# Optimization experiments

Hardware: AMD Instinct MI355X
Metric: run time of the kernel (lower is better)

## Reference

```python
import jax, jax.numpy as jnp
import numpy as np

NEG_SLOPE = 0.01  # torch leaky_relu default

def leaky_relu(x):
    return jnp.where(x >= 0, x, NEG_SLOPE * x)

def setup_inputs() -> dict:
    key = jax.random.key(0)
    ks = jax.random.split(key, 12)
    N, E = 100000, 800000
    C_in, C_edge, pre, H, hs, C_out = 64, 32, 96, 4, 24, 128
    aggr_out = H * hs + 1  # count=True appends in-degree column
    x = jax.random.normal(ks[0], (N, C_in), dtype=jnp.float32)
    edge_attr = jax.random.normal(ks[1], (E, C_edge), dtype=jnp.float32)
    edge_index = jax.random.randint(ks[2], (2, E), 0, N, dtype=jnp.int32)
    s = 0.05
    W_pre = jax.random.normal(ks[3], (C_in + C_edge, pre), dtype=jnp.float32) * s
    b_pre = jax.random.normal(ks[4], (pre,), dtype=jnp.float32) * s
    W_att = jax.random.normal(ks[5], (pre, H), dtype=jnp.float32) * s
    b_att = jax.random.normal(ks[6], (H,), dtype=jnp.float32) * s
    W_val = jax.random.normal(ks[7], (pre, H * hs), dtype=jnp.float32) * s
    b_val = jax.random.normal(ks[8], (H * hs,), dtype=jnp.float32) * s
    W_out = jax.random.normal(ks[9], (C_in + aggr_out, C_out), dtype=jnp.float32) * s
    b_out = jax.random.normal(ks[10], (C_out,), dtype=jnp.float32) * s
    return {"x": x, "edge_attr": edge_attr, "edge_index": edge_index,
            "W_pre": W_pre, "b_pre": b_pre, "W_att": W_att, "b_att": b_att,
            "W_val": W_val, "b_val": b_val, "W_out": W_out, "b_out": b_out}

def reference(x, edge_attr, edge_index, W_pre, b_pre, W_att, b_att, W_val, b_val, W_out, b_out):
    N = x.shape[0]
    src, dst = edge_index[0], edge_index[1]
    H = W_att.shape[1]
    hs = W_val.shape[1] // H
    # gather + pre MLP: [E, in+edge] -> [E, pre]
    msg = jnp.concatenate([x[src], edge_attr], axis=-1)
    msg = leaky_relu(msg @ W_pre + b_pre)
    # multi-head attention aggregation keyed by destination
    logits = msg @ W_att + b_att                       # [E, H]
    vals = (msg @ W_val + b_val).reshape(-1, H, hs)    # [E, H, hs]
    seg_max = jax.ops.segment_max(logits, dst, num_segments=N)      # [N, H]
    seg_max = jnp.where(jnp.isfinite(seg_max), seg_max, 0.0)
    alpha = jnp.exp(logits - seg_max[dst])                          # [E, H]
    denom = jax.ops.segment_sum(alpha, dst, num_segments=N)         # [N, H]
    alpha = alpha / denom[dst]
    agg = jax.ops.segment_sum(alpha[:, :, None] * vals, dst, num_segments=N)  # [N, H, hs]
    agg = agg.reshape(N, H * hs)
    count = jax.ops.segment_sum(jnp.ones((src.shape[0], 1), dtype=x.dtype), dst, num_segments=N)
    messages = jnp.concatenate([agg, count], axis=-1)
    out = jnp.concatenate([x, messages], axis=-1)
    return leaky_relu(out @ W_out + b_out)
```

## Files before the change

### kernel.cpp

```cpp
#include <hip/hip_runtime.h>


#define NEG 0.01f

__device__ __forceinline__ float lrelu(float v) { return v > 0.f ? v : NEG * v; }

__device__ __forceinline__ unsigned bfpack2(float a, float b) {
    unsigned ua = __float_as_uint(a); ua = (ua + 0x7fff + ((ua >> 16) & 1)) >> 16;
    unsigned ub = __float_as_uint(b); ub = (ub + 0x7fff + ((ub >> 16) & 1)) >> 16;
    return ua | (ub << 16);
}

__global__ void zero_kernel(float* __restrict__ p, long n) {
    long i = ((long)blockIdx.x * 256 + threadIdx.x) * 4;
    if (i + 3 < n) {
        *(float4*)(p + i) = make_float4(0.f, 0.f, 0.f, 0.f);
    } else {
        for (long k = i; k < n; ++k) p[k] = 0.f;
    }
}

__global__ void hist_kernel(const int* __restrict__ ei, int* __restrict__ cnt, int E) {
    int e = blockIdx.x * 256 + threadIdx.x;
    if (e < E) atomicAdd(&cnt[ei[E + e]], 1);
}

__global__ __launch_bounds__(1024)
void scan_kernel(const int* __restrict__ cnt, int* __restrict__ offs,
                 int* __restrict__ curs, int N) {
    __shared__ int ls[1024];
    int tid = threadIdx.x;
    int chunk = (N + 1023) >> 10;
    int lo = tid * chunk;
    int hi = lo + chunk; if (hi > N) hi = N; if (lo > N) lo = N;
    int s = 0;
    for (int i = lo; i < hi; ++i) s += cnt[i];
    ls[tid] = s;
    __syncthreads();
    for (int off = 1; off < 1024; off <<= 1) {
        int v = 0;
        if (tid >= off) v = ls[tid - off];
        __syncthreads();
        ls[tid] += v;
        __syncthreads();
    }
    int run = ls[tid] - s;
    for (int i = lo; i < hi; ++i) {
        offs[i] = run; curs[i] = run; run += cnt[i];
    }
}

__global__ __launch_bounds__(256)
void blocksum_kernel(const int* __restrict__ cnt, int* __restrict__ bsum, int N) {
    int base = blockIdx.x * 1024;
    int tid = threadIdx.x;
    int v = 0;
#pragma unroll
    for (int r = 0; r < 4; ++r) {
        int idx = base + r * 256 + tid;
        if (idx < N) v += cnt[idx];
    }
#pragma unroll
    for (int d = 32; d > 0; d >>= 1) v += __shfl_down(v, d, 64);
    __shared__ int ws[4];
    int wv = tid >> 6, lane = tid & 63;
    if (lane == 0) ws[wv] = v;
    __syncthreads();
    if (tid == 0) bsum[blockIdx.x] = ws[0] + ws[1] + ws[2] + ws[3];
}

__global__ __launch_bounds__(1024)
void bscan_kernel(int* __restrict__ bsum, int NB) {
    __shared__ int ls[1024];
    int tid = threadIdx.x;
    int v = (tid < NB) ? bsum[tid] : 0;
    ls[tid] = v;
    __syncthreads();
    for (int off = 1; off < 1024; off <<= 1) {
        int t = 0;
        if (tid >= off) t = ls[tid - off];
        __syncthreads();
        ls[tid] += t;
        __syncthreads();
    }
    if (tid < NB) bsum[tid] = ls[tid] - v;
}

__global__ __launch_bounds__(1024)
void offs_kernel(const int* __restrict__ cnt, const int* __restrict__ boff,
                 int* __restrict__ offs, int* __restrict__ curs, int N) {
    int tid = threadIdx.x;
    int i = blockIdx.x * 1024 + tid;
    int lane = tid & 63, wv = tid >> 6;
    int c = (i < N) ? cnt[i] : 0;
    int v = c;
#pragma unroll
    for (int d = 1; d < 64; d <<= 1) {
        int t = __shfl_up(v, d, 64);
        if (lane >= d) v += t;
    }
    __shared__ int ws[16];
    if (lane == 63) ws[wv] = v;
    __syncthreads();
    if (wv == 0) {
        int wvv = (lane < 16) ? ws[lane] : 0;
#pragma unroll
        for (int d = 1; d < 16; d <<= 1) {
            int t = __shfl_up(wvv, d, 64);
            if (lane >= d) wvv += t;
        }
        if (lane < 16) ws[lane] = wvv;
    }
    __syncthreads();
    int waveoff = (wv > 0) ? ws[wv - 1] : 0;
    int excl = v - c + waveoff + boff[blockIdx.x];
    if (i < N) { offs[i] = excl; curs[i] = excl; }
}

__global__ __launch_bounds__(256, 4)
void pre_kernel(const float* __restrict__ x, const float* __restrict__ Wp,
                const float* __restrict__ bp, float* __restrict__ U, int N)
{
    __shared__ float xs[64][65];
    int n0 = blockIdx.x * 64;
    for (int p = threadIdx.x; p < 64 * 16; p += 256) {
        int row = p >> 4, f4 = p & 15;
        int n = n0 + row;
        float4 v = make_float4(0.f, 0.f, 0.f, 0.f);
        if (n < N) v = ((const float4*)(x + (long)n * 64))[f4];
        xs[row][f4 * 4 + 0] = v.x; xs[row][f4 * 4 + 1] = v.y;
        xs[row][f4 * 4 + 2] = v.z; xs[row][f4 * 4 + 3] = v.w;
    }
    __syncthreads();

    int node = threadIdx.x >> 2;
    int cg = threadIdx.x & 3;
    float4 acc[6];
#pragma unroll
    for (int c = 0; c < 6; ++c) acc[c] = ((const float4*)(bp + cg * 24))[c];
    for (int k = 0; k < 64; ++k) {
        float xv = xs[node][k];
        const float* wr = Wp + k * 96 + cg * 24;
#pragma unroll
        for (int c = 0; c < 6; ++c) {
            float4 w = ((const float4*)wr)[c];
            acc[c].x += xv * w.x; acc[c].y += xv * w.y;
            acc[c].z += xv * w.z; acc[c].w += xv * w.w;
        }
    }
    int n = n0 + node;
    if (n < N) {
#pragma unroll
        for (int c = 0; c < 6; ++c)
            ((float4*)(U + (long)n * 96 + cg * 24))[c] = acc[c];
    }
}

__global__ __launch_bounds__(256, 1)
void edge_msg_kernel(const float* __restrict__ U, const float* __restrict__ ea,
                     const int* __restrict__ ei,
                     const float* __restrict__ Wp,
                     const float* __restrict__ Wa, const float* __restrict__ ba,
                     unsigned* __restrict__ vals, int* __restrict__ curs, int E)
{
    __shared__ __attribute__((aligned(16))) float WpS[32 * 96];
    __shared__ __attribute__((aligned(16))) float WaS[96 * 4];

    const float* Wp2 = Wp + 64 * 96;
    for (int i = threadIdx.x; i < 32 * 24; i += 256)
        ((float4*)WpS)[i] = ((const float4*)Wp2)[i];
    for (int i = threadIdx.x; i < 96; i += 256)
        ((float4*)WaS)[i] = ((const float4*)Wa)[i];
    __syncthreads();

    int t = blockIdx.x * 256 + threadIdx.x;
    int e = t >> 1;
    int half = t & 1;
    int lane = threadIdx.x & 63;
    bool active = (e < E);
    int ec = active ? e : (E - 1);
    int src = ei[ec];
    int dst = ei[E + ec];

    int pos = 0;
    if (active && half == 0) pos = atomicAdd(&curs[dst], 1);

    float4 S[12];
    const float4* Urow = (const float4*)(U + (long)src * 96) + half * 12;
#pragma unroll
    for (int j = 0; j < 12; ++j) S[j] = Urow[j];

    const float* erow = ea + (long)ec * 32;
    const float4* WpS4 = (const float4*)WpS;

#pragma unroll 1
    for (int kc = 0; kc < 8; ++kc) {
        float4 c = ((const float4*)erow)[kc];
        const float4* w0 = WpS4 + (4 * kc + 0) * 24 + half * 12;
        const float4* w1 = WpS4 + (4 * kc + 1) * 24 + half * 12;
        const float4* w2 = WpS4 + (4 * kc + 2) * 24 + half * 12;
        const float4* w3 = WpS4 + (4 * kc + 3) * 24 + half * 12;
#pragma unroll
        for (int j = 0; j < 12; ++j) {
            float4 a0 = w0[j], a1 = w1[j], a2 = w2[j], a3 = w3[j];
            S[j].x += c.x * a0.x + c.y * a1.x + c.z * a2.x + c.w * a3.x;
            S[j].y += c.x * a0.y + c.y * a1.y + c.z * a2.y + c.w * a3.y;
            S[j].z += c.x * a0.z + c.y * a1.z + c.z * a2.z + c.w * a3.z;
            S[j].w += c.x * a0.w + c.y * a1.w + c.z * a2.w + c.w * a3.w;
        }
    }
#pragma unroll
    for (int j = 0; j < 12; ++j) {
        S[j].x = lrelu(S[j].x); S[j].y = lrelu(S[j].y);
        S[j].z = lrelu(S[j].z); S[j].w = lrelu(S[j].w);
    }

    float l0 = 0.f, l1 = 0.f, l2 = 0.f, l3 = 0.f;
    const float4* WaS4 = (const float4*)WaS;
#pragma unroll
    for (int j = 0; j < 12; ++j) {
        float4 m = S[j];
        const float4* war = WaS4 + half * 48 + 4 * j;
        float4 w0 = war[0], w1 = war[1], w2 = war[2], w3 = war[3];
        l0 += m.x * w0.x + m.y * w1.x + m.z * w2.x + m.w * w3.x;
        l1 += m.x * w0.y + m.y * w1.y + m.z * w2.y + m.w * w3.y;
        l2 += m.x * w0.z + m.y * w1.z + m.z * w2.z + m.w * w3.z;
        l3 += m.x * w0.w + m.y * w1.w + m.z * w2.w + m.w * w3.w;
    }
    l0 += __shfl_xor(l0, 1, 64);
    l1 += __shfl_xor(l1, 1, 64);
    l2 += __shfl_xor(l2, 1, 64);
    l3 += __shfl_xor(l3, 1, 64);

    pos = __shfl(pos, lane & 62, 64);

    if (active) {
        unsigned* rowb = vals + (long)pos * 52;
        unsigned* row = rowb + half * 24;
#pragma unroll
        for (int j2 = 0; j2 < 6; ++j2) {
            uint4 u;
            u.x = bfpack2(S[2 * j2].x,     S[2 * j2].y);
            u.y = bfpack2(S[2 * j2].z,     S[2 * j2].w);
            u.z = bfpack2(S[2 * j2 + 1].x, S[2 * j2 + 1].y);
            u.w = bfpack2(S[2 * j2 + 1].z, S[2 * j2 + 1].w);
            ((uint4*)row)[j2] = u;
        }
        if (half) {
            float p0 = __expf(l0 + ba[0]), p1 = __expf(l1 + ba[1]);
            float p2 = __expf(l2 + ba[2]), p3 = __expf(l3 + ba[3]);
            ((uint4*)rowb)[12] = make_uint4(__float_as_uint(p0), __float_as_uint(p1),
                                            __float_as_uint(p2), __float_as_uint(p3));
        }
    }
}

__global__ __launch_bounds__(512)
void gather_kernel(const unsigned* __restrict__ vals, const int* __restrict__ offs,
                   const int* __restrict__ cnt,
                   const float* __restrict__ Wv, const float* __restrict__ bv,
                   float* __restrict__ agg, float* __restrict__ cntF, int N)
{
    __shared__ __attribute__((aligned(16))) float Wvs[96][96];
    __shared__ float Tls[8][4][96];
    int wv = threadIdx.x >> 6;
    int lane = threadIdx.x & 63;
    int node = blockIdx.x * 8 + wv;
    bool nvalid = (node < N);

    for (int i = threadIdx.x; i < 96 * 24; i += 512)
        ((float4*)Wvs)[i] = ((const float4*)Wv)[i];
    __syncthreads();

    int start = nvalid ? offs[node] : 0;
    int deg   = nvalid ? cnt[node] : 0;

    float s0[4] = {0.f, 0.f, 0.f, 0.f};
    float s1[4] = {0.f, 0.f, 0.f, 0.f};
    float d0 = 0.f, d1 = 0.f, d2 = 0.f, d3 = 0.f;
    if (lane < 52) {
#define PROC(v) {                                                   \
        float vf = __uint_as_float(v);                              \
        float q0 = __shfl(vf, 48, 64);                              \
        float q1 = __shfl(vf, 49, 64);                              \
        float q2 = __shfl(vf, 50, 64);                              \
        float q3 = __shfl(vf, 51, 64);                              \
        float m0 = __uint_as_float((v) << 16);                      \
        float m1 = __uint_as_float((v) & 0xffff0000u);              \
        s0[0] += q0 * m0; s1[0] += q0 * m1;                         \
        s0[1] += q1 * m0; s1[1] += q1 * m1;                         \
        s0[2] += q2 * m0; s1[2] += q2 * m1;                         \
        s0[3] += q3 * m0; s1[3] += q3 * m1;                         \
        d0 += q0; d1 += q1; d2 += q2; d3 += q3; }
        const unsigned* p = vals + (long)start * 52 + lane;
        int r = 0;
        for (; r + 4 <= deg; r += 4, p += 208) {
            unsigned va = p[0];
            unsigned vb = p[52];
            unsigned vc = p[104];
            unsigned vd = p[156];
            PROC(va) PROC(vb) PROC(vc) PROC(vd)
        }
        for (; r < deg; ++r, p += 52) {
            unsigned v = *p;
            PROC(v)
        }
#undef PROC
    }
    if (lane < 48) {
        float r0 = (deg > 0) ? 1.f / d0 : 0.f;
        float r1 = (deg > 0) ? 1.f / d1 : 0.f;
        float r2 = (deg > 0) ? 1.f / d2 : 0.f;
        float r3 = (deg > 0) ? 1.f / d3 : 0.f;
        Tls[wv][0][2 * lane] = s0[0] * r0; Tls[wv][0][2 * lane + 1] = s1[0] * r0;
        Tls[wv][1][2 * lane] = s0[1] * r1; Tls[wv][1][2 * lane + 1] = s1[1] * r1;
        Tls[wv][2][2 * lane] = s0[2] * r2; Tls[wv][2][2 * lane + 1] = s1[2] * r2;
        Tls[wv][3][2 * lane] = s0[3] * r3; Tls[wv][3][2 * lane + 1] = s1[3] * r3;
    }
    if (nvalid) {
        if (lane < 48) {
            int j = 2 * lane;
            int h = lane / 12;
            float a0 = bv[j], a1 = bv[j + 1];
            const float* Th = &Tls[wv][h][0];
#pragma unroll 4
            for (int k = 0; k < 96; ++k) {
                float t = Th[k];
                float2 w = *(const float2*)&Wvs[k][j];
                a0 += t * w.x; a1 += t * w.y;
            }
            float2 o = (deg > 0) ? make_float2(a0, a1) : make_float2(0.f, 0.f);
            *(float2*)(agg + (long)node * 96 + j) = o;
        } else if (lane == 48) {
            cntF[node] = (float)deg;
        }
    }
}

__global__ __launch_bounds__(256, 4)
void node_kernel(const float* __restrict__ x, const float* __restrict__ aggW,
                 const float* __restrict__ cntF,
                 const float* __restrict__ Wo, const float* __restrict__ bo,
                 float* __restrict__ out, int N)
{
    __shared__ float s_in[161][68];
    int n0 = blockIdx.x * 64;
    int j0 = blockIdx.y * 64;

    for (int idx = threadIdx.x; idx < 64 * 16; idx += 256) {
        int row = idx >> 4, f4 = idx & 15;
        int n = n0 + row;
        float4 v = make_float4(0.f, 0.f, 0.f, 0.f);
        if (n < N) v = ((const float4*)(x + (long)n * 64))[f4];
        s_in[4 * f4 + 0][row] = v.x; s_in[4 * f4 + 1][row] = v.y;
        s_in[4 * f4 + 2][row] = v.z; s_in[4 * f4 + 3][row] = v.w;
    }
    for (int idx = threadIdx.x; idx < 64 * 24; idx += 256) {
        int row = idx / 24, c4 = idx % 24;
        int n = n0 + row;
        float4 v = make_float4(0.f, 0.f, 0.f, 0.f);
        if (n < N) v = ((const float4*)(aggW + (long)n * 96))[c4];
        s_in[64 + 4 * c4 + 0][row] = v.x; s_in[64 + 4 * c4 + 1][row] = v.y;
        s_in[64 + 4 * c4 + 2][row] = v.z; s_in[64 + 4 * c4 + 3][row] = v.w;
    }
    if (threadIdx.x < 64) {
        int n = n0 + threadIdx.x;
        s_in[160][threadIdx.x] = (n < N) ? cntF[n] : 0.f;
    }
    __syncthreads();

    int tj = threadIdx.x & 15;
    int tn = threadIdx.x >> 4;
    float acc[4][4];
#pragma unroll
    for (int i = 0; i < 4; ++i)
#pragma unroll
        for (int c = 0; c < 4; ++c) acc[i][c] = 0.f;

    const float* Wcol = Wo + j0 + tj * 4;
    for (int k = 0; k < 161; ++k) {
        float4 w  = *(const float4*)(Wcol + (long)k * 128);
        float4 iv = *(const float4*)&s_in[k][tn * 4];
        acc[0][0] += iv.x * w.x; acc[0][1] += iv.x * w.y; acc[0][2] += iv.x * w.z; acc[0][3] += iv.x * w.w;
        acc[1][0] += iv.y * w.x; acc[1][1] += iv.y * w.y; acc[1][2] += iv.y * w.z; acc[1][3] += iv.y * w.w;
        acc[2][0] += iv.z * w.x; acc[2][1] += iv.z * w.y; acc[2][2] += iv.z * w.z; acc[2][3] += iv.z * w.w;
        acc[3][0] += iv.w * w.x; acc[3][1] += iv.w * w.y; acc[3][2] += iv.w * w.z; acc[3][3] += iv.w * w.w;
    }
    float4 b = *(const float4*)(bo + j0 + tj * 4);
#pragma unroll
    for (int i = 0; i < 4; ++i) {
        int n = n0 + tn * 4 + i;
        if (n < N) {
            float4 o;
            o.x = lrelu(acc[i][0] + b.x);
            o.y = lrelu(acc[i][1] + b.y);
            o.z = lrelu(acc[i][2] + b.z);
            o.w = lrelu(acc[i][3] + b.w);
            *(float4*)(out + (long)n * 128 + j0 + tj * 4) = o;
        }
    }
}

__global__ __launch_bounds__(256, 1)
void edge_atm_kernel(const float* __restrict__ x, const float* __restrict__ ea,
                     const int* __restrict__ ei,
                     const float* __restrict__ Wp, const float* __restrict__ bp,
                     const float* __restrict__ Wa, const float* __restrict__ ba,
                     const float* __restrict__ Wv, const float* __restrict__ bv,
                     float* __restrict__ aggW, float* __restrict__ denomW,
                     float* __restrict__ cntW, int E)
{
    int e = blockIdx.x * 256 + threadIdx.x;
    if (e >= E) return;
    int src = ei[e];
    int dst = ei[E + e];
    float4 S[24];
#pragma unroll
    for (int j = 0; j < 24; ++j) S[j] = ((const float4*)bp)[j];
    const float* xrow = x + (long)src * 64;
    const float* erow = ea + (long)e * 32;
#pragma unroll 1
    for (int kc = 0; kc < 6; ++kc) {
        const float* sp = (kc < 4) ? (xrow + kc * 16) : (erow + (kc - 4) * 16);
        const float* Wb = Wp + kc * 16 * 96;
#pragma unroll 1
        for (int i = 0; i < 4; ++i) {
            float4 cc = ((const float4*)sp)[i];
#pragma unroll
            for (int j = 0; j < 24; ++j) {
                float4 w0 = ((const float4*)(Wb + (4 * i + 0) * 96))[j];
                float4 w1 = ((const float4*)(Wb + (4 * i + 1) * 96))[j];
                float4 w2 = ((const float4*)(Wb + (4 * i + 2) * 96))[j];
                float4 w3 = ((const float4*)(Wb + (4 * i + 3) * 96))[j];
                S[j].x += cc.x * w0.x + cc.y * w1.x + cc.z * w2.x + cc.w * w3.x;
                S[j].y += cc.x * w0.y + cc.y * w1.y + cc.z * w2.y + cc.w * w3.y;
                S[j].z += cc.x * w0.z + cc.y * w1.z + cc.z * w2.z + cc.w * w3.z;
                S[j].w += cc.x * w0.w + cc.y * w1.w + cc.z * w2.w + cc.w * w3.w;
            }
        }
    }
#pragma unroll
    for (int j = 0; j < 24; ++j) {
        S[j].x = lrelu(S[j].x); S[j].y = lrelu(S[j].y);
        S[j].z = lrelu(S[j].z); S[j].w = lrelu(S[j].w);
    }
    float l0 = ba[0], l1 = ba[1], l2 = ba[2], l3 = ba[3];
#pragma unroll
    for (int j = 0; j < 24; ++j) {
        float4 m = S[j];
        float4 w0 = ((const float4*)(Wa + (4 * j + 0) * 4))[0];
        float4 w1 = ((const float4*)(Wa + (4 * j + 1) * 4))[0];
        float4 w2 = ((const float4*)(Wa + (4 * j + 2) * 4))[0];
        float4 w3 = ((const float4*)(Wa + (4 * j + 3) * 4))[0];
        l0 += m.x * w0.x + m.y * w1.x + m.z * w2.x + m.w * w3.x;
        l1 += m.x * w0.y + m.y * w1.y + m.z * w2.y + m.w * w3.y;
        l2 += m.x * w0.z + m.y * w1.z + m.z * w2.z + m.w * w3.z;
        l3 += m.x * w0.w + m.y * w1.w + m.z * w2.w + m.w * w3.w;
    }
    float p0 = __expf(l0), p1 = __expf(l1), p2 = __expf(l2), p3 = __expf(l3);
    float* aggp = aggW + (long)dst * 96;
#pragma unroll 1
    for (int j4 = 0; j4 < 24; ++j4) {
        float4 acc = ((const float4*)bv)[j4];
        const float* Wc = Wv + 4 * j4;
#pragma unroll
        for (int j = 0; j < 24; ++j) {
            float4 m = S[j];
            float4 w0 = ((const float4*)(Wc + (4 * j + 0) * 96))[0];
            float4 w1 = ((const float4*)(Wc + (4 * j + 1) * 96))[0];
            float4 w2 = ((const float4*)(Wc + (4 * j + 2) * 96))[0];
            float4 w3 = ((const float4*)(Wc + (4 * j + 3) * 96))[0];
            acc.x += m.x * w0.x + m.y * w1.x + m.z * w2.x + m.w * w3.x;
            acc.y += m.x * w0.y + m.y * w1.y + m.z * w2.y + m.w * w3.y;
            acc.z += m.x * w0.z + m.y * w1.z + m.z * w2.z + m.w * w3.z;
            acc.w += m.x * w0.w + m.y * w1.w + m.z * w2.w + m.w * w3.w;
        }
        float ph = (j4 < 6) ? p0 : (j4 < 12) ? p1 : (j4 < 18) ? p2 : p3;
        unsafeAtomicAdd(aggp + 4 * j4 + 0, ph * acc.x);
        unsafeAtomicAdd(aggp + 4 * j4 + 1, ph * acc.y);
        unsafeAtomicAdd(aggp + 4 * j4 + 2, ph * acc.z);
        unsafeAtomicAdd(aggp + 4 * j4 + 3, ph * acc.w);
    }
    float* dn = denomW + (long)dst * 4;
    unsafeAtomicAdd(dn + 0, p0);
    unsafeAtomicAdd(dn + 1, p1);
    unsafeAtomicAdd(dn + 2, p2);
    unsafeAtomicAdd(dn + 3, p3);
    unsafeAtomicAdd(cntW + dst, 1.0f);
}

__global__ __launch_bounds__(256, 4)
void node_atm_kernel(const float* __restrict__ x, const float* __restrict__ aggW,
                     const float* __restrict__ denomW, const float* __restrict__ cntW,
                     const float* __restrict__ Wo, const float* __restrict__ bo,
                     float* __restrict__ out, int N)
{
    __shared__ float s_in[161][64];
    int n0 = blockIdx.x * 64;
    int j0 = blockIdx.y * 64;
    for (int p = threadIdx.x; p < 161 * 64; p += 256) {
        int k = p >> 6, nl = p & 63;
        int n = n0 + nl;
        float v = 0.f;
        if (n < N) {
            if (k < 64) v = x[(long)n * 64 + k];
            else if (k < 160) {
                int kk = k - 64;
                float d = denomW[n * 4 + (kk / 24)];
                v = d > 0.f ? aggW[(long)n * 96 + kk] / d : 0.f;
            } else v = cntW[n];
        }
        s_in[k][nl] = v;
    }
    __syncthreads();
    int tj = threadIdx.x & 15;
    int tn = threadIdx.x >> 4;
    float acc[4][4];
#pragma unroll
    for (int i = 0; i < 4; ++i)
#pragma unroll
        for (int c = 0; c < 4; ++c) acc[i][c] = 0.f;
    const float* Wcol = Wo + j0 + tj * 4;
    for (int k = 0; k < 161; ++k) {
        float4 w  = *(const float4*)(Wcol + (long)k * 128);
        float4 iv = *(const float4*)&s_in[k][tn * 4];
        acc[0][0] += iv.x * w.x; acc[0][1] += iv.x * w.y; acc[0][2] += iv.x * w.z; acc[0][3] += iv.x * w.w;
        acc[1][0] += iv.y * w.x; acc[1][1] += iv.y * w.y; acc[1][2] += iv.y * w.z; acc[1][3] += iv.y * w.w;
        acc[2][0] += iv.z * w.x; acc[2][1] += iv.z * w.y; acc[2][2] += iv.z * w.z; acc[2][3] += iv.z * w.w;
        acc[3][0] += iv.w * w.x; acc[3][1] += iv.w * w.y; acc[3][2] += iv.w * w.z; acc[3][3] += iv.w * w.w;
    }
    float4 b = *(const float4*)(bo + j0 + tj * 4);
#pragma unroll
    for (int i = 0; i < 4; ++i) {
        int n = n0 + tn * 4 + i;
        if (n < N) {
            float4 o;
            o.x = lrelu(acc[i][0] + b.x);
            o.y = lrelu(acc[i][1] + b.y);
            o.z = lrelu(acc[i][2] + b.z);
            o.w = lrelu(acc[i][3] + b.w);
            *(float4*)(out + (long)n * 128 + j0 + tj * 4) = o;
        }
    }
}

extern "C" void kernel_launch(void* const* d_in, const int* in_sizes, int n_in,
                              void* d_out, int out_size, void* d_ws, size_t ws_size,
                              hipStream_t stream)
{
    const float* x  = (const float*)d_in[0];
    const float* ea = (const float*)d_in[1];
    const int*   ei = (const int*)d_in[2];
    const float* Wp = (const float*)d_in[3];
    const float* bp = (const float*)d_in[4];
    const float* Wa = (const float*)d_in[5];
    const float* ba = (const float*)d_in[6];
    const float* Wv = (const float*)d_in[7];
    const float* bv = (const float*)d_in[8];
    const float* Wo = (const float*)d_in[9];
    const float* bo = (const float*)d_in[10];
    float* out = (float*)d_out;

    int N = in_sizes[0] / 64;
    int E = in_sizes[2] / 2;
    int NB = (N + 1023) / 1024;

    size_t need = (size_t)E * 52 * 4 + (size_t)N * 96 * 4 + (size_t)N * 4 * 4
                + (size_t)NB * 4;

    if (ws_size >= need) {
        unsigned* vals = (unsigned*)d_ws;
        float* Uagg = (float*)(vals + (long)E * 52);
        float* cntF = Uagg + (long)N * 96;
        int*   cnti = (int*)(cntF + N);
        int*   offs = cnti + N;
        int*   curs = offs + N;
        int*   bsum = curs + N;

        hipMemsetAsync(cnti, 0, (size_t)N * sizeof(int), stream);
        hist_kernel<<<(E + 255) / 256, 256, 0, stream>>>(ei, cnti, E);
        if (NB <= 1024) {
            blocksum_kernel<<<NB, 256, 0, stream>>>(cnti, bsum, N);
            bscan_kernel<<<1, 1024, 0, stream>>>(bsum, NB);
            offs_kernel<<<NB, 1024, 0, stream>>>(cnti, bsum, offs, curs, N);
        } else {
            scan_kernel<<<1, 1024, 0, stream>>>(cnti, offs, curs, N);
        }
        pre_kernel<<<(N + 63) / 64, 256, 0, stream>>>(x, Wp, bp, Uagg, N);
        edge_msg_kernel<<<(2 * E + 255) / 256, 256, 0, stream>>>(
            Uagg, ea, ei, Wp, Wa, ba, vals, curs, E);
        gather_kernel<<<(N + 7) / 8, 512, 0, stream>>>(
            vals, offs, cnti, Wv, bv, Uagg, cntF, N);
        dim3 ng((N + 63) / 64, 2);
        node_kernel<<<ng, 256, 0, stream>>>(x, Uagg, cntF, Wo, bo, out, N);
    } else {
        float* aggW   = (float*)d_ws;
        float* denomW = aggW + (long)N * 96;
        float* cntW   = denomW + (long)N * 4;
        long zn = (long)N * 101;
        int  zb = (int)(((zn + 3) / 4 + 255) / 256);
        zero_kernel<<<zb, 256, 0, stream>>>(aggW, zn);
        edge_atm_kernel<<<(E + 255) / 256, 256, 0, stream>>>(
            x, ea, ei, Wp, bp, Wa, ba, Wv, bv, aggW, denomW, cntW, E);
        dim3 ng((N + 63) / 64, 2);
        node_atm_kernel<<<ng, 256, 0, stream>>>(x, aggW, denomW, cntW, Wo, bo, out, N);
    }
}
```

Measured before the change: 736.6 us.

## Split edge work across wavefronts so weight loads become wave-uniform scalar loads

The edge message kernel now assigns each wavefront one half of the 96 output features for 64 edges, so the half index is wave-uniform. Weight rows are read straight from global memory with uniform addresses, which lets the compiler use scalar loads instead of staging Wp and Wa in LDS, and removes the block-wide weight preload. The cross-half reduction of attention logits and the sharing of the scatter position now go through a small LDS exchange with a __syncthreads instead of lane shuffles. In exchange, each thread's edge_attr and U row reads are less coalesced across the wave pair, and a block barrier is added partway through the kernel.

```diff
diff --git a/kernel.cpp b/kernel.cpp
--- a/kernel.cpp
+++ b/kernel.cpp
@@ -163,50 +163,46 @@
                      const float* __restrict__ Wa, const float* __restrict__ ba,
                      unsigned* __restrict__ vals, int* __restrict__ curs, int E)
 {
-    __shared__ __attribute__((aligned(16))) float WpS[32 * 96];
-    __shared__ __attribute__((aligned(16))) float WaS[96 * 4];
-
-    const float* Wp2 = Wp + 64 * 96;
-    for (int i = threadIdx.x; i < 32 * 24; i += 256)
-        ((float4*)WpS)[i] = ((const float4*)Wp2)[i];
-    for (int i = threadIdx.x; i < 96; i += 256)
-        ((float4*)WaS)[i] = ((const float4*)Wa)[i];
-    __syncthreads();
-
-    int t = blockIdx.x * 256 + threadIdx.x;
-    int e = t >> 1;
-    int half = t & 1;
+    __shared__ float ex[5][2][64];
+
     int lane = threadIdx.x & 63;
+    int wid  = threadIdx.x >> 6;
+    int half = __builtin_amdgcn_readfirstlane(wid & 1);
+    int pl   = __builtin_amdgcn_readfirstlane(wid >> 1);
+    int e = (blockIdx.x * 2 + pl) * 64 + lane;
     bool active = (e < E);
     int ec = active ? e : (E - 1);
     int src = ei[ec];
     int dst = ei[E + ec];
 
     int pos = 0;
-    if (active && half == 0) pos = atomicAdd(&curs[dst], 1);
+    if (half == 0 && active) pos = atomicAdd(&curs[dst], 1);
 
     float4 S[12];
-    const float4* Urow = (const float4*)(U + (long)src * 96) + half * 12;
+    const float4* Urow = (const float4*)(U + (long)src * 96 + half * 48);
 #pragma unroll
     for (int j = 0; j < 12; ++j) S[j] = Urow[j];
 
     const float* erow = ea + (long)ec * 32;
-    const float4* WpS4 = (const float4*)WpS;
+    const float* Wh = Wp + 64 * 96 + half * 48;
 
 #pragma unroll 1
     for (int kc = 0; kc < 8; ++kc) {
         float4 c = ((const float4*)erow)[kc];
-        const float4* w0 = WpS4 + (4 * kc + 0) * 24 + half * 12;
-        const float4* w1 = WpS4 + (4 * kc + 1) * 24 + half * 12;
-        const float4* w2 = WpS4 + (4 * kc + 2) * 24 + half * 12;
-        const float4* w3 = WpS4 + (4 * kc + 3) * 24 + half * 12;
+        const float* W0 = Wh + (4 * kc + 0) * 96;
+        const float* W1 = Wh + (4 * kc + 1) * 96;
+        const float* W2 = Wh + (4 * kc + 2) * 96;
+        const float* W3 = Wh + (4 * kc + 3) * 96;
 #pragma unroll
         for (int j = 0; j < 12; ++j) {
-            float4 a0 = w0[j], a1 = w1[j], a2 = w2[j], a3 = w3[j];
-            S[j].x += c.x * a0.x + c.y * a1.x + c.z * a2.x + c.w * a3.x;
-            S[j].y += c.x * a0.y + c.y * a1.y + c.z * a2.y + c.w * a3.y;
-            S[j].z += c.x * a0.z + c.y * a1.z + c.z * a2.z + c.w * a3.z;
-            S[j].w += c.x * a0.w + c.y * a1.w + c.z * a2.w + c.w * a3.w;
+            float4 w0 = ((const float4*)W0)[j];
+            float4 w1 = ((const float4*)W1)[j];
+            float4 w2 = ((const float4*)W2)[j];
+            float4 w3 = ((const float4*)W3)[j];
+            S[j].x += c.x * w0.x + c.y * w1.x + c.z * w2.x + c.w * w3.x;
+            S[j].y += c.x * w0.y + c.y * w1.y + c.z * w2.y + c.w * w3.y;
+            S[j].z += c.x * w0.z + c.y * w1.z + c.z * w2.z + c.w * w3.z;
+            S[j].w += c.x * w0.w + c.y * w1.w + c.z * w2.w + c.w * w3.w;
         }
     }
 #pragma unroll
@@ -216,23 +212,31 @@
     }
 
     float l0 = 0.f, l1 = 0.f, l2 = 0.f, l3 = 0.f;
-    const float4* WaS4 = (const float4*)WaS;
+    const float* Wah = Wa + half * 48 * 4;
 #pragma unroll
     for (int j = 0; j < 12; ++j) {
         float4 m = S[j];
-        const float4* war = WaS4 + half * 48 + 4 * j;
-        float4 w0 = war[0], w1 = war[1], w2 = war[2], w3 = war[3];
+        float4 w0 = ((const float4*)(Wah + (4 * j + 0) * 4))[0];
+        float4 w1 = ((const float4*)(Wah + (4 * j + 1) * 4))[0];
+        float4 w2 = ((const float4*)(Wah + (4 * j + 2) * 4))[0];
+        float4 w3 = ((const float4*)(Wah + (4 * j + 3) * 4))[0];
         l0 += m.x * w0.x + m.y * w1.x + m.z * w2.x + m.w * w3.x;
         l1 += m.x * w0.y + m.y * w1.y + m.z * w2.y + m.w * w3.y;
         l2 += m.x * w0.z + m.y * w1.z + m.z * w2.z + m.w * w3.z;
         l3 += m.x * w0.w + m.y * w1.w + m.z * w2.w + m.w * w3.w;
     }
-    l0 += __shfl_xor(l0, 1, 64);
-    l1 += __shfl_xor(l1, 1, 64);
-    l2 += __shfl_xor(l2, 1, 64);
-    l3 += __shfl_xor(l3, 1, 64);
-
-    pos = __shfl(pos, lane & 62, 64);
+
+    if (half == 0) {
+        ex[0][pl][lane] = __int_as_float(pos);
+        ex[1][pl][lane] = l0; ex[2][pl][lane] = l1;
+        ex[3][pl][lane] = l2; ex[4][pl][lane] = l3;
+    }
+    __syncthreads();
+    if (half == 1) {
+        pos = __float_as_int(ex[0][pl][lane]);
+        l0 += ex[1][pl][lane]; l1 += ex[2][pl][lane];
+        l2 += ex[3][pl][lane]; l3 += ex[4][pl][lane];
+    }
 
     if (active) {
         unsigned* rowb = vals + (long)pos * 52;
@@ -246,7 +250,7 @@
             u.w = bfpack2(S[2 * j2 + 1].z, S[2 * j2 + 1].w);
             ((uint4*)row)[j2] = u;
         }
-        if (half) {
+        if (half == 1) {
             float p0 = __expf(l0 + ba[0]), p1 = __expf(l1 + ba[1]);
             float p2 = __expf(l2 + ba[2]), p3 = __expf(l3 + ba[3]);
             ((uint4*)rowb)[12] = make_uint4(__float_as_uint(p0), __float_as_uint(p1),
```

Result: no change. 745.2 us (+1.2%).
